# Optimization experiments

Hardware: AMD Instinct MI355X
Metric: run time of the kernel (lower is better)

Reference implementation:

```python
import jax, jax.numpy as jnp
import numpy as np

N = 100000   # nodes
E = 1600000  # edges (avg degree 16)
IN, H, OUT, P = 100, 256, 256, 128
EPS = 1e-5


def setup_inputs() -> dict:
    key = jax.random.key(0)
    ks = jax.random.split(key, 12)

    def lin(k, o, i):
        return jax.random.normal(k, (o, i), jnp.float32) / np.float32(np.sqrt(i))

    return {
        "x": jax.random.normal(ks[0], (N, IN), jnp.float32),
        "edge_index": jax.random.randint(ks[1], (2, E), 0, N),
        # SAGEConv l (aggregated-neighbor branch, has bias) and r (root branch, no bias)
        "Wl0": lin(ks[2], H, IN), "bl0": jnp.zeros((H,), jnp.float32), "Wr0": lin(ks[3], H, IN),
        "Wl1": lin(ks[4], H, H),  "bl1": jnp.zeros((H,), jnp.float32), "Wr1": lin(ks[5], H, H),
        "Wl2": lin(ks[6], OUT, H), "bl2": jnp.zeros((OUT,), jnp.float32), "Wr2": lin(ks[7], OUT, H),
        # projection head + BatchNorm1d(128)
        "Wp": lin(ks[8], P, OUT), "bp": jnp.zeros((P,), jnp.float32),
        "gamma": jnp.ones((P,), jnp.float32), "beta": jnp.zeros((P,), jnp.float32),
    }


def _sage_conv(x, src, dst, Wl, bl, Wr):
    # PyG SAGEConv default: mean-aggregate source features into destinations,
    # then lin_l(agg) + lin_r(x).
    agg = jax.ops.segment_sum(x[src], dst, num_segments=N)           # [N, d]
    deg = jax.ops.segment_sum(jnp.ones((src.shape[0],), x.dtype), dst, num_segments=N)
    agg = agg / jnp.maximum(deg, 1.0)[:, None]
    return agg @ Wl.T + bl + x @ Wr.T


def reference(x, edge_index, Wl0, bl0, Wr0, Wl1, bl1, Wr1, Wl2, bl2, Wr2, Wp, bp, gamma, beta):
    src, dst = edge_index[0], edge_index[1]
    x = jax.nn.relu(_sage_conv(x, src, dst, Wl0, bl0, Wr0))  # dropout is identity in eval
    x = jax.nn.relu(_sage_conv(x, src, dst, Wl1, bl1, Wr1))
    x = _sage_conv(x, src, dst, Wl2, bl2, Wr2)               # no relu on last layer
    z = x @ Wp.T + bp                                        # projection head -> [N, 128]
    mu = jnp.mean(z, axis=0)
    var = jnp.var(z, axis=0)                                 # biased, as torch BN uses for normalization
    h = gamma * (z - mu) * jax.lax.rsqrt(var + EPS) + beta
    return (x, h)
```

## Files before the change

### kernel.cpp

```cpp
#include <hip/hip_runtime.h>
#include <hip/hip_bf16.h>

#define EPS_BN 1e-5f

using short8  = __attribute__((ext_vector_type(8))) short;
using ushort8 = __attribute__((ext_vector_type(8))) unsigned short;
using f32x4   = __attribute__((ext_vector_type(4))) float;

__device__ inline float bf2f(unsigned short u) {
    union { unsigned i; float f; } c; c.i = ((unsigned)u) << 16; return c.f;
}
__device__ inline unsigned short f2bf(float f) {
    unsigned x = __float_as_uint(f);
    unsigned r = (x + 0x7FFF + ((x >> 16) & 1)) >> 16;
    return (unsigned short)r;
}

__global__ void zero_i32(int* __restrict__ p, int n) {
    int i = blockIdx.x * blockDim.x + threadIdx.x;
    if (i < n) p[i] = 0;
}
__global__ void zero_f32(float* __restrict__ p, int n) {
    int i = blockIdx.x * blockDim.x + threadIdx.x;
    if (i < n) p[i] = 0.0f;
}

__global__ void conv_w(const float* __restrict__ w, unsigned short* __restrict__ o,
                       int R, int C, int CP) {
    int t = blockIdx.x * blockDim.x + threadIdx.x;
    if (t >= R * CP) return;
    int r = t / CP, c = t % CP;
    o[t] = (c < C) ? f2bf(w[(size_t)r * C + c]) : (unsigned short)0;
}

__global__ void conv_x_pad(const float* __restrict__ x, unsigned short* __restrict__ xp, int n) {
    int t = blockIdx.x * blockDim.x + threadIdx.x;
    if (t >= n * 32) return;
    int node = t >> 5, g = t & 31;
    int f0 = g * 4;
    ushort4 o;
    const float* xr = x + (size_t)node * 100;
    o.x = (f0 + 0 < 100) ? f2bf(xr[f0 + 0]) : 0;
    o.y = (f0 + 1 < 100) ? f2bf(xr[f0 + 1]) : 0;
    o.z = (f0 + 2 < 100) ? f2bf(xr[f0 + 2]) : 0;
    o.w = (f0 + 3 < 100) ? f2bf(xr[f0 + 3]) : 0;
    *(ushort4*)(xp + (size_t)node * 128 + f0) = o;
}

__global__ void count_k(const int* __restrict__ dst, int* __restrict__ counts, int E) {
    int i = blockIdx.x * blockDim.x + threadIdx.x;
    if (i < E) atomicAdd(&counts[dst[i]], 1);
}

__global__ void scan1(const int* __restrict__ counts, int* __restrict__ rp,
                      int* __restrict__ partials, int n) {
    __shared__ int s[256];
    int t = threadIdx.x;
    int i = blockIdx.x * 256 + t;
    int v = (i < n) ? counts[i] : 0;
    s[t] = v;
    __syncthreads();
    for (int off = 1; off < 256; off <<= 1) {
        int u = (t >= off) ? s[t - off] : 0;
        __syncthreads();
        s[t] += u;
        __syncthreads();
    }
    if (i < n) rp[i] = s[t] - v;
    if (t == 255) partials[blockIdx.x] = s[255];
}

__global__ void scan2(int* __restrict__ partials, int nb) {
    __shared__ int s[512];
    int t = threadIdx.x;
    int v = (t < nb) ? partials[t] : 0;
    s[t] = v;
    __syncthreads();
    for (int off = 1; off < 512; off <<= 1) {
        int u = (t >= off) ? s[t - off] : 0;
        __syncthreads();
        s[t] += u;
        __syncthreads();
    }
    if (t < nb) partials[t] = s[t] - v;
}

__global__ void scan3(int* __restrict__ rp, const int* __restrict__ partials, int n, int E) {
    int i = blockIdx.x * blockDim.x + threadIdx.x;
    if (i < n) rp[i] += partials[i >> 8];
    if (i == 0) rp[n] = E;
}

__global__ void fill_k(const int* __restrict__ src, const int* __restrict__ dst,
                       const int* __restrict__ rp, int* __restrict__ cursor,
                       int* __restrict__ col, int E) {
    int i = blockIdx.x * blockDim.x + threadIdx.x;
    if (i < E) {
        int d = dst[i];
        int pos = atomicAdd(&cursor[d], 1);
        col[rp[d] + pos] = src[i];
    }
}

__global__ __launch_bounds__(256) void agg_bf16_256(
    const unsigned short* __restrict__ x, const int* __restrict__ rp,
    const int* __restrict__ col, unsigned short* __restrict__ out, int n) {
    int wave = threadIdx.x >> 6, lane = threadIdx.x & 63;
    int node = blockIdx.x * 4 + wave;
    if (node >= n) return;
    int s = rp[node], e = rp[node + 1];
    int deg = e - s;
    int h = lane >> 5;
    int l32 = lane & 31;

    float a[8] = {0, 0, 0, 0, 0, 0, 0, 0};
    int base = 0;
    for (; base + 8 <= deg; base += 8) {
        int i = s + base + h;
        int r0 = col[i], r1 = col[i + 2], r2 = col[i + 4], r3 = col[i + 6];
        ushort8 v0 = *(const ushort8*)(x + (size_t)r0 * 256 + l32 * 8);
        ushort8 v1 = *(const ushort8*)(x + (size_t)r1 * 256 + l32 * 8);
        ushort8 v2 = *(const ushort8*)(x + (size_t)r2 * 256 + l32 * 8);
        ushort8 v3 = *(const ushort8*)(x + (size_t)r3 * 256 + l32 * 8);
#pragma unroll
        for (int j = 0; j < 8; ++j)
            a[j] += bf2f(v0[j]) + bf2f(v1[j]) + bf2f(v2[j]) + bf2f(v3[j]);
    }
    for (int i = s + base + h; i < e; i += 2) {
        int r = col[i];
        ushort8 v = *(const ushort8*)(x + (size_t)r * 256 + l32 * 8);
#pragma unroll
        for (int j = 0; j < 8; ++j) a[j] += bf2f(v[j]);
    }
#pragma unroll
    for (int j = 0; j < 8; ++j) a[j] += __shfl_xor(a[j], 32);

    if (h == 0) {
        float sc = 1.0f / fmaxf((float)deg, 1.0f);
        ushort8 o;
#pragma unroll
        for (int j = 0; j < 8; ++j) o[j] = f2bf(a[j] * sc);
        *(ushort8*)(out + (size_t)node * 256 + l32 * 8) = o;
    }
}

__global__ __launch_bounds__(256) void agg_bf16_128(
    const unsigned short* __restrict__ x, const int* __restrict__ rp,
    const int* __restrict__ col, unsigned short* __restrict__ out, int n) {
    int wave = threadIdx.x >> 6, lane = threadIdx.x & 63;
    int node = blockIdx.x * 4 + wave;
    if (node >= n) return;
    int s = rp[node], e = rp[node + 1];
    int deg = e - s;
    int q = lane >> 4;
    int l16 = lane & 15;

    float a[8] = {0, 0, 0, 0, 0, 0, 0, 0};
    int base = 0;
    for (; base + 16 <= deg; base += 16) {
        int i = s + base + q;
        int r0 = col[i], r1 = col[i + 4], r2 = col[i + 8], r3 = col[i + 12];
        ushort8 v0 = *(const ushort8*)(x + (size_t)r0 * 128 + l16 * 8);
        ushort8 v1 = *(const ushort8*)(x + (size_t)r1 * 128 + l16 * 8);
        ushort8 v2 = *(const ushort8*)(x + (size_t)r2 * 128 + l16 * 8);
        ushort8 v3 = *(const ushort8*)(x + (size_t)r3 * 128 + l16 * 8);
#pragma unroll
        for (int j = 0; j < 8; ++j)
            a[j] += bf2f(v0[j]) + bf2f(v1[j]) + bf2f(v2[j]) + bf2f(v3[j]);
    }
    for (int i = s + base + q; i < e; i += 4) {
        int r = col[i];
        ushort8 v = *(const ushort8*)(x + (size_t)r * 128 + l16 * 8);
#pragma unroll
        for (int j = 0; j < 8; ++j) a[j] += bf2f(v[j]);
    }
#pragma unroll
    for (int j = 0; j < 8; ++j) {
        a[j] += __shfl_xor(a[j], 16);
        a[j] += __shfl_xor(a[j], 32);
    }

    if (lane < 16) {
        float sc = 1.0f / fmaxf((float)deg, 1.0f);
        ushort8 o;
#pragma unroll
        for (int j = 0; j < 8; ++j) o[j] = f2bf(a[j] * sc);
        *(ushort8*)(out + (size_t)node * 128 + l16 * 8) = o;
    }
}

template <int KTOT, int DOUT, bool HAS_AGG, bool RELU, bool STF32, bool STBF16>
__global__ __launch_bounds__(256) void sage_mfma(
    const unsigned short* __restrict__ xp, const unsigned short* __restrict__ ap,
    const unsigned short* __restrict__ Wr, const unsigned short* __restrict__ Wl,
    const float* __restrict__ bias,
    float* __restrict__ outf, unsigned short* __restrict__ outb, int n) {
    constexpr int CT = DOUT / 16;
    constexpr int NSRC = HAS_AGG ? 2 : 1;
    constexpr int FR = DOUT * 4;
    __shared__ __align__(16) unsigned short lds[NSRC * FR * 8];

    const int t = threadIdx.x;
    const int wave = t >> 6, lane = t & 63;
    const int node0 = blockIdx.x * 64 + wave * 16;
    const bool active = node0 < n;
    const int lcol = lane & 15, lq = lane >> 4;

    f32x4 acc[CT];
#pragma unroll
    for (int c = 0; c < CT; ++c) {
        float b = bias[c * 16 + lcol];
        acc[c][0] = b; acc[c][1] = b; acc[c][2] = b; acc[c][3] = b;
    }

    const unsigned short* aRow  = xp + (size_t)(node0 + lcol) * KTOT + lq * 8;
    const unsigned short* aRow2 = HAS_AGG ? (ap + (size_t)(node0 + lcol) * KTOT + lq * 8) : xp;

    for (int ks = 0; ks < KTOT / 32; ++ks) {
        for (int r = t; r < NSRC * FR; r += 256) {
            int srcSel = r / FR;
            int id = r % FR;
            int ct = id >> 6, l = id & 63;
            const unsigned short* W = (srcSel == 0) ? Wr : Wl;
            uint4 v = *(const uint4*)(W + (size_t)(ct * 16 + (l & 15)) * KTOT + ks * 32 + (l >> 4) * 8);
            *(uint4*)(lds + (size_t)r * 8) = v;
        }
        __syncthreads();
        if (active) {
            short8 a = *(const short8*)(aRow + ks * 32);
            short8 a2;
            if (HAS_AGG) a2 = *(const short8*)(aRow2 + ks * 32);
            const short8* bf = (const short8*)lds;
#pragma unroll
            for (int c = 0; c < CT; ++c)
                acc[c] = __builtin_amdgcn_mfma_f32_16x16x32_bf16(a, bf[c * 64 + lane], acc[c], 0, 0, 0);
            if (HAS_AGG) {
                const short8* bf2 = bf + FR;
#pragma unroll
                for (int c = 0; c < CT; ++c)
                    acc[c] = __builtin_amdgcn_mfma_f32_16x16x32_bf16(a2, bf2[c * 64 + lane], acc[c], 0, 0, 0);
            }
        }
        __syncthreads();
    }
    if (!active) return;

#pragma unroll
    for (int c = 0; c < CT; ++c) {
        f32x4 v = acc[c];
        if (RELU) {
            v[0] = fmaxf(v[0], 0.0f); v[1] = fmaxf(v[1], 0.0f);
            v[2] = fmaxf(v[2], 0.0f); v[3] = fmaxf(v[3], 0.0f);
        }
#pragma unroll
        for (int j = 0; j < 4; ++j) {
            size_t row = (size_t)node0 + lq * 4 + j;
            int colI = c * 16 + lcol;
            if (STF32) outf[row * DOUT + colI] = v[j];
            if (STBF16) outb[row * DOUT + colI] = f2bf(v[j]);
        }
    }
}

__global__ void bn_partial(const float* __restrict__ z, float* __restrict__ sums, int n) {
    int f = threadIdx.x & 127;
    int half = threadIdx.x >> 7;
    float s = 0.0f, s2 = 0.0f;
    for (int row = blockIdx.x * 2 + half; row < n; row += gridDim.x * 2) {
        float v = z[(size_t)row * 128 + f];
        s += v; s2 += v * v;
    }
    __shared__ float ls[256], ls2[256];
    ls[threadIdx.x] = s; ls2[threadIdx.x] = s2;
    __syncthreads();
    if (half == 0) {
        atomicAdd(&sums[f], s + ls[128 + f]);
        atomicAdd(&sums[128 + f], s2 + ls2[128 + f]);
    }
}

__global__ void bn_finalize(const float* __restrict__ sums, const float* __restrict__ gamma,
                            const float* __restrict__ beta, float* __restrict__ params, int n) {
    int f = threadIdx.x;
    float mu = sums[f] / (float)n;
    float var = sums[128 + f] / (float)n - mu * mu;
    float inv = rsqrtf(var + EPS_BN);
    float sc = gamma[f] * inv;
    params[f] = sc;
    params[128 + f] = beta[f] - mu * sc;
}

__global__ void bn_apply(float* __restrict__ z, const float* __restrict__ params, int total4) {
    int i = blockIdx.x * blockDim.x + threadIdx.x;
    for (; i < total4; i += gridDim.x * blockDim.x) {
        float4 v = ((float4*)z)[i];
        int f0 = (i & 31) * 4;
        v.x = v.x * params[f0 + 0] + params[128 + f0 + 0];
        v.y = v.y * params[f0 + 1] + params[128 + f0 + 1];
        v.z = v.z * params[f0 + 2] + params[128 + f0 + 2];
        v.w = v.w * params[f0 + 3] + params[128 + f0 + 3];
        ((float4*)z)[i] = v;
    }
}

extern "C" void kernel_launch(void* const* d_in, const int* in_sizes, int n_in,
                              void* d_out, int out_size, void* d_ws, size_t ws_size,
                              hipStream_t stream) {
    const float* x_in  = (const float*)d_in[0];
    const int*   ei    = (const int*)d_in[1];
    const float* Wl0   = (const float*)d_in[2];
    const float* bl0   = (const float*)d_in[3];
    const float* Wr0   = (const float*)d_in[4];
    const float* Wl1   = (const float*)d_in[5];
    const float* bl1   = (const float*)d_in[6];
    const float* Wr1   = (const float*)d_in[7];
    const float* Wl2   = (const float*)d_in[8];
    const float* bl2   = (const float*)d_in[9];
    const float* Wr2   = (const float*)d_in[10];
    const float* Wp    = (const float*)d_in[11];
    const float* bp    = (const float*)d_in[12];
    const float* gamma = (const float*)d_in[13];
    const float* beta  = (const float*)d_in[14];

    const int IN = 100, INP = 128, H = 256, OUT = 256, P = 128;
    const int n = in_sizes[0] / IN;
    const int E = in_sizes[1] / 2;
    const int* src = ei;
    const int* dst = ei + E;

    size_t off = 0;
    auto alloc = [&](size_t bytes) -> char* {
        char* p = (char*)d_ws + off;
        off += (bytes + 255) & ~(size_t)255;
        return p;
    };
    int*   counts   = (int*)alloc((size_t)n * 4);
    int*   cursor   = (int*)alloc((size_t)n * 4);
    int*   rp       = (int*)alloc((size_t)(n + 1) * 4);
    int*   partials = (int*)alloc(512 * 4);
    int*   col      = (int*)alloc((size_t)E * 4);
    unsigned short* Wl0b = (unsigned short*)alloc((size_t)H * INP * 2);
    unsigned short* Wr0b = (unsigned short*)alloc((size_t)H * INP * 2);
    unsigned short* Wl1b = (unsigned short*)alloc((size_t)H * H * 2);
    unsigned short* Wr1b = (unsigned short*)alloc((size_t)H * H * 2);
    unsigned short* Wl2b = (unsigned short*)alloc((size_t)OUT * H * 2);
    unsigned short* Wr2b = (unsigned short*)alloc((size_t)OUT * H * 2);
    unsigned short* Wpb  = (unsigned short*)alloc((size_t)P * OUT * 2);
    float* bnsums   = (float*)alloc(256 * 4);
    float* bnparams = (float*)alloc(256 * 4);
    unsigned short* bufA = (unsigned short*)alloc((size_t)n * H * 2);
    unsigned short* bufB = (unsigned short*)alloc((size_t)n * H * 2);
    unsigned short* bufC = (unsigned short*)alloc((size_t)n * H * 2);
    unsigned short* bufD = (unsigned short*)alloc((size_t)n * H * 2);

    unsigned short* xpad   = bufA;
    unsigned short* aggpad = bufA + (size_t)n * INP;
    unsigned short* h1b  = bufB;
    unsigned short* agg1 = bufC;
    unsigned short* h2b  = bufD;
    unsigned short* agg2 = bufB;
    unsigned short* xb2  = bufA;

    float* out_x = (float*)d_out;
    float* z     = out_x + (size_t)n * OUT;

    const int nb = (n + 255) / 256;
    const int gemm_grid = (n + 63) / 64;

    zero_i32<<<nb, 256, 0, stream>>>(counts, n);
    zero_i32<<<nb, 256, 0, stream>>>(cursor, n);
    zero_f32<<<1, 256, 0, stream>>>(bnsums, 256);
    count_k<<<(E + 255) / 256, 256, 0, stream>>>(dst, counts, E);
    scan1<<<nb, 256, 0, stream>>>(counts, rp, partials, n);
    scan2<<<1, 512, 0, stream>>>(partials, nb);
    scan3<<<nb, 256, 0, stream>>>(rp, partials, n, E);
    fill_k<<<(E + 255) / 256, 256, 0, stream>>>(src, dst, rp, cursor, col, E);

    conv_x_pad<<<(n * 32 + 255) / 256, 256, 0, stream>>>(x_in, xpad, n);
    conv_w<<<(H * INP + 255) / 256, 256, 0, stream>>>(Wl0, Wl0b, H, IN, INP);
    conv_w<<<(H * INP + 255) / 256, 256, 0, stream>>>(Wr0, Wr0b, H, IN, INP);
    conv_w<<<(H * H + 255) / 256, 256, 0, stream>>>(Wl1, Wl1b, H, H, H);
    conv_w<<<(H * H + 255) / 256, 256, 0, stream>>>(Wr1, Wr1b, H, H, H);
    conv_w<<<(OUT * H + 255) / 256, 256, 0, stream>>>(Wl2, Wl2b, OUT, H, H);
    conv_w<<<(OUT * H + 255) / 256, 256, 0, stream>>>(Wr2, Wr2b, OUT, H, H);
    conv_w<<<(P * OUT + 255) / 256, 256, 0, stream>>>(Wp, Wpb, P, OUT, OUT);

    agg_bf16_128<<<(n + 3) / 4, 256, 0, stream>>>(xpad, rp, col, aggpad, n);
    sage_mfma<128, 256, true, true, false, true><<<gemm_grid, 256, 0, stream>>>(
        xpad, aggpad, Wr0b, Wl0b, bl0, nullptr, h1b, n);

    agg_bf16_256<<<(n + 3) / 4, 256, 0, stream>>>(h1b, rp, col, agg1, n);
    sage_mfma<256, 256, true, true, false, true><<<gemm_grid, 256, 0, stream>>>(
        h1b, agg1, Wr1b, Wl1b, bl1, nullptr, h2b, n);

    agg_bf16_256<<<(n + 3) / 4, 256, 0, stream>>>(h2b, rp, col, agg2, n);
    sage_mfma<256, 256, true, false, true, true><<<gemm_grid, 256, 0, stream>>>(
        h2b, agg2, Wr2b, Wl2b, bl2, out_x, xb2, n);

    sage_mfma<256, 128, false, false, true, false><<<gemm_grid, 256, 0, stream>>>(
        xb2, nullptr, Wpb, nullptr, bp, z, nullptr, n);

    bn_partial<<<256, 256, 0, stream>>>(z, bnsums, n);
    bn_finalize<<<1, 128, 0, stream>>>(bnsums, gamma, beta, bnparams, n);
    bn_apply<<<2048, 256, 0, stream>>>(z, bnparams, n * (P / 4));
}
```

Measured before the change: 821.8 us.

## Double-buffer weight staging via direct global-to-LDS loads and 512-thread GEMM blocks

Rewrites the weight staging in the SAGE MFMA GEMM so each wave issues direct global-to-LDS loads into a double-buffered shared tile, prefetching the next k-slice while the current one is consumed. Blocks grow to 512 threads covering 128 nodes, which halves how often each weight slice is reloaded per node. It also defers the aggregate-row load until just before use. The loop still needs a sync before the next buffer is overwritten, and the larger LDS footprint (two buffers) may reduce occupancy.

```diff
diff --git a/kernel.cpp b/kernel.cpp
--- a/kernel.cpp
+++ b/kernel.cpp
@@ -6,6 +6,9 @@
 using short8  = __attribute__((ext_vector_type(8))) short;
 using ushort8 = __attribute__((ext_vector_type(8))) unsigned short;
 using f32x4   = __attribute__((ext_vector_type(4))) float;
+
+typedef const __attribute__((address_space(1))) void* gas_ptr;
+typedef __attribute__((address_space(3))) void* las_ptr;
 
 __device__ inline float bf2f(unsigned short u) {
     union { unsigned i; float f; } c; c.i = ((unsigned)u) << 16; return c.f;
@@ -190,21 +193,38 @@
 }
 
 template <int KTOT, int DOUT, bool HAS_AGG, bool RELU, bool STF32, bool STBF16>
-__global__ __launch_bounds__(256) void sage_mfma(
+__global__ __launch_bounds__(512) void sage_mfma(
     const unsigned short* __restrict__ xp, const unsigned short* __restrict__ ap,
     const unsigned short* __restrict__ Wr, const unsigned short* __restrict__ Wl,
     const float* __restrict__ bias,
     float* __restrict__ outf, unsigned short* __restrict__ outb, int n) {
     constexpr int CT = DOUT / 16;
     constexpr int NSRC = HAS_AGG ? 2 : 1;
-    constexpr int FR = DOUT * 4;
-    __shared__ __align__(16) unsigned short lds[NSRC * FR * 8];
+    constexpr int FR = NSRC == 2 ? DOUT * 4 : DOUT * 4;
+    constexpr int CHUNKS = NSRC * CT;
+    constexpr int CPW = CHUNKS / 8;
+    constexpr int KS = KTOT / 32;
+    constexpr int BUFSZ = NSRC * FR * 8;
+    __shared__ __align__(16) unsigned short lds[2 * BUFSZ];
 
     const int t = threadIdx.x;
     const int wave = t >> 6, lane = t & 63;
-    const int node0 = blockIdx.x * 64 + wave * 16;
+    const int node0 = blockIdx.x * 128 + wave * 16;
     const bool active = node0 < n;
     const int lcol = lane & 15, lq = lane >> 4;
+
+    auto stage = [&](int ks, int buf) {
+        unsigned short* base = lds + buf * BUFSZ;
+#pragma unroll
+        for (int i = 0; i < CPW; ++i) {
+            int chunk = wave * CPW + i;
+            int srcSel = chunk / CT, ct = chunk % CT;
+            const unsigned short* W = (srcSel == 0) ? Wr : Wl;
+            const unsigned short* g = W + (size_t)(ct * 16 + lcol) * KTOT + ks * 32 + lq * 8;
+            unsigned short* l = base + chunk * 512;
+            __builtin_amdgcn_global_load_lds((gas_ptr)g, (las_ptr)l, 16, 0, 0);
+        }
+    };
 
     f32x4 acc[CT];
 #pragma unroll
@@ -216,25 +236,19 @@
     const unsigned short* aRow  = xp + (size_t)(node0 + lcol) * KTOT + lq * 8;
     const unsigned short* aRow2 = HAS_AGG ? (ap + (size_t)(node0 + lcol) * KTOT + lq * 8) : xp;
 
-    for (int ks = 0; ks < KTOT / 32; ++ks) {
-        for (int r = t; r < NSRC * FR; r += 256) {
-            int srcSel = r / FR;
-            int id = r % FR;
-            int ct = id >> 6, l = id & 63;
-            const unsigned short* W = (srcSel == 0) ? Wr : Wl;
-            uint4 v = *(const uint4*)(W + (size_t)(ct * 16 + (l & 15)) * KTOT + ks * 32 + (l >> 4) * 8);
-            *(uint4*)(lds + (size_t)r * 8) = v;
-        }
-        __syncthreads();
+    stage(0, 0);
+    __syncthreads();
+
+    for (int ks = 0; ks < KS; ++ks) {
+        if (ks + 1 < KS) stage(ks + 1, (ks + 1) & 1);
         if (active) {
             short8 a = *(const short8*)(aRow + ks * 32);
-            short8 a2;
-            if (HAS_AGG) a2 = *(const short8*)(aRow2 + ks * 32);
-            const short8* bf = (const short8*)lds;
+            const short8* bf = (const short8*)(lds + (ks & 1) * BUFSZ);
 #pragma unroll
             for (int c = 0; c < CT; ++c)
                 acc[c] = __builtin_amdgcn_mfma_f32_16x16x32_bf16(a, bf[c * 64 + lane], acc[c], 0, 0, 0);
             if (HAS_AGG) {
+                short8 a2 = *(const short8*)(aRow2 + ks * 32);
                 const short8* bf2 = bf + FR;
 #pragma unroll
                 for (int c = 0; c < CT; ++c)
@@ -365,7 +379,7 @@
     float* z     = out_x + (size_t)n * OUT;
 
     const int nb = (n + 255) / 256;
-    const int gemm_grid = (n + 63) / 64;
+    const int gemm_grid = (n + 127) / 128;
 
     zero_i32<<<nb, 256, 0, stream>>>(counts, n);
     zero_i32<<<nb, 256, 0, stream>>>(cursor, n);
@@ -386,18 +400,18 @@
     conv_w<<<(P * OUT + 255) / 256, 256, 0, stream>>>(Wp, Wpb, P, OUT, OUT);
 
     agg_bf16_128<<<(n + 3) / 4, 256, 0, stream>>>(xpad, rp, col, aggpad, n);
-    sage_mfma<128, 256, true, true, false, true><<<gemm_grid, 256, 0, stream>>>(
+    sage_mfma<128, 256, true, true, false, true><<<gemm_grid, 512, 0, stream>>>(
         xpad, aggpad, Wr0b, Wl0b, bl0, nullptr, h1b, n);
 
     agg_bf16_256<<<(n + 3) / 4, 256, 0, stream>>>(h1b, rp, col, agg1, n);
-    sage_mfma<256, 256, true, true, false, true><<<gemm_grid, 256, 0, stream>>>(
+    sage_mfma<256, 256, true, true, false, true><<<gemm_grid, 512, 0, stream>>>(
         h1b, agg1, Wr1b, Wl1b, bl1, nullptr, h2b, n);
 
     agg_bf16_256<<<(n + 3) / 4, 256, 0, stream>>>(h2b, rp, col, agg2, n);
-    sage_mfma<256, 256, true, false, true, true><<<gemm_grid, 256, 0, stream>>>(
+    sage_mfma<256, 256, true, false, true, true><<<gemm_grid, 512, 0, stream>>>(
         h2b, agg2, Wr2b, Wl2b, bl2, out_x, xb2, n);
 
-    sage_mfma<256, 128, false, false, true, false><<<gemm_grid, 256, 0, stream>>>(
+    sage_mfma<256, 128, false, false, true, false><<<gemm_grid, 512, 0, stream>>>(
         xb2, nullptr, Wpb, nullptr, bp, z, nullptr, n);
 
     bn_partial<<<256, 256, 0, stream>>>(z, bnsums, n);
```

Measured after the change: 742.4 us. -9.7%, faster.

## Register-tile SAGE GEMMs with 64x64 per-wave tiles and double-buffered direct loads

Applied to the files above, without the earlier changes.

Replaces the LDS-staged weight GEMM, where each wave computed a 16-row strip across all output columns, with 512-thread blocks in which each wave owns a 64x64 output tile. A and B fragments are loaded straight from global memory into registers and double-buffered across k-steps, which removes the shared-memory staging and both __syncthreads per k-step. The aim is more MFMA work per loaded fragment and fewer block-level barriers. In exchange, register pressure is much higher (16 accumulators plus two sets of operand fragments), weights are read repeatedly from global or L2 memory, and occupancy may drop.

```diff
diff --git a/kernel.cpp b/kernel.cpp
--- a/kernel.cpp
+++ b/kernel.cpp
@@ -189,75 +189,106 @@
     }
 }
 
-template <int KTOT, int DOUT, bool HAS_AGG, bool RELU, bool STF32, bool STBF16>
-__global__ __launch_bounds__(256) void sage_mfma(
+template <int KTOT, int DOUT, bool HAS_AGG, bool RELU, bool STF32, bool STBF16, int WAVES_M>
+__global__ __launch_bounds__(512) void sage_mfma(
     const unsigned short* __restrict__ xp, const unsigned short* __restrict__ ap,
     const unsigned short* __restrict__ Wr, const unsigned short* __restrict__ Wl,
     const float* __restrict__ bias,
     float* __restrict__ outf, unsigned short* __restrict__ outb, int n) {
-    constexpr int CT = DOUT / 16;
-    constexpr int NSRC = HAS_AGG ? 2 : 1;
-    constexpr int FR = DOUT * 4;
-    __shared__ __align__(16) unsigned short lds[NSRC * FR * 8];
+    constexpr int WAVES_N = 8 / WAVES_M;
+    constexpr int KS = KTOT / 32;
+    static_assert(DOUT / 16 / WAVES_N == 4, "wave owns 4 col tiles");
 
     const int t = threadIdx.x;
     const int wave = t >> 6, lane = t & 63;
-    const int node0 = blockIdx.x * 64 + wave * 16;
-    const bool active = node0 < n;
+    const int wm = wave / WAVES_N, wn = wave % WAVES_N;
     const int lcol = lane & 15, lq = lane >> 4;
-
-    f32x4 acc[CT];
-#pragma unroll
-    for (int c = 0; c < CT; ++c) {
-        float b = bias[c * 16 + lcol];
-        acc[c][0] = b; acc[c][1] = b; acc[c][2] = b; acc[c][3] = b;
-    }
-
-    const unsigned short* aRow  = xp + (size_t)(node0 + lcol) * KTOT + lq * 8;
-    const unsigned short* aRow2 = HAS_AGG ? (ap + (size_t)(node0 + lcol) * KTOT + lq * 8) : xp;
-
-    for (int ks = 0; ks < KTOT / 32; ++ks) {
-        for (int r = t; r < NSRC * FR; r += 256) {
-            int srcSel = r / FR;
-            int id = r % FR;
-            int ct = id >> 6, l = id & 63;
-            const unsigned short* W = (srcSel == 0) ? Wr : Wl;
-            uint4 v = *(const uint4*)(W + (size_t)(ct * 16 + (l & 15)) * KTOT + ks * 32 + (l >> 4) * 8);
-            *(uint4*)(lds + (size_t)r * 8) = v;
+    const int node_base = blockIdx.x * (WAVES_M * 64) + wm * 64;
+    const int col0 = wn * 64;
+
+    f32x4 acc[4][4];
+#pragma unroll
+    for (int ct = 0; ct < 4; ++ct) {
+        float b = bias[col0 + ct * 16 + lcol];
+#pragma unroll
+        for (int mt = 0; mt < 4; ++mt) {
+            acc[mt][ct][0] = b; acc[mt][ct][1] = b; acc[mt][ct][2] = b; acc[mt][ct][3] = b;
         }
-        __syncthreads();
-        if (active) {
-            short8 a = *(const short8*)(aRow + ks * 32);
-            short8 a2;
-            if (HAS_AGG) a2 = *(const short8*)(aRow2 + ks * 32);
-            const short8* bf = (const short8*)lds;
-#pragma unroll
-            for (int c = 0; c < CT; ++c)
-                acc[c] = __builtin_amdgcn_mfma_f32_16x16x32_bf16(a, bf[c * 64 + lane], acc[c], 0, 0, 0);
-            if (HAS_AGG) {
-                const short8* bf2 = bf + FR;
-#pragma unroll
-                for (int c = 0; c < CT; ++c)
-                    acc[c] = __builtin_amdgcn_mfma_f32_16x16x32_bf16(a2, bf2[c * 64 + lane], acc[c], 0, 0, 0);
+    }
+
+    const unsigned short* aPx[4];
+    const unsigned short* aPa[4];
+    const unsigned short* bPr[4];
+    const unsigned short* bPl[4];
+#pragma unroll
+    for (int i = 0; i < 4; ++i) {
+        aPx[i] = xp + (size_t)(node_base + i * 16 + lcol) * KTOT + lq * 8;
+        bPr[i] = Wr + (size_t)(col0 + i * 16 + lcol) * KTOT + lq * 8;
+        if (HAS_AGG) {
+            aPa[i] = ap + (size_t)(node_base + i * 16 + lcol) * KTOT + lq * 8;
+            bPl[i] = Wl + (size_t)(col0 + i * 16 + lcol) * KTOT + lq * 8;
+        }
+    }
+
+    short8 axE[4], aaE[4], brE[4], blE[4];
+    short8 axO[4], aaO[4], brO[4], blO[4];
+
+    auto LOAD = [&](int ks, short8 (&ax)[4], short8 (&aa)[4],
+                    short8 (&br)[4], short8 (&bl)[4]) {
+#pragma unroll
+        for (int i = 0; i < 4; ++i) {
+            ax[i] = *(const short8*)(aPx[i] + ks * 32);
+            br[i] = *(const short8*)(bPr[i] + ks * 32);
+        }
+        if constexpr (HAS_AGG) {
+#pragma unroll
+            for (int i = 0; i < 4; ++i) {
+                aa[i] = *(const short8*)(aPa[i] + ks * 32);
+                bl[i] = *(const short8*)(bPl[i] + ks * 32);
             }
         }
-        __syncthreads();
-    }
-    if (!active) return;
-
-#pragma unroll
-    for (int c = 0; c < CT; ++c) {
-        f32x4 v = acc[c];
-        if (RELU) {
-            v[0] = fmaxf(v[0], 0.0f); v[1] = fmaxf(v[1], 0.0f);
-            v[2] = fmaxf(v[2], 0.0f); v[3] = fmaxf(v[3], 0.0f);
-        }
-#pragma unroll
-        for (int j = 0; j < 4; ++j) {
-            size_t row = (size_t)node0 + lq * 4 + j;
-            int colI = c * 16 + lcol;
-            if (STF32) outf[row * DOUT + colI] = v[j];
-            if (STBF16) outb[row * DOUT + colI] = f2bf(v[j]);
+    };
+    auto MM = [&](short8 (&ax)[4], short8 (&aa)[4],
+                  short8 (&br)[4], short8 (&bl)[4]) {
+#pragma unroll
+        for (int mt = 0; mt < 4; ++mt)
+#pragma unroll
+            for (int ct = 0; ct < 4; ++ct) {
+                acc[mt][ct] = __builtin_amdgcn_mfma_f32_16x16x32_bf16(
+                    ax[mt], br[ct], acc[mt][ct], 0, 0, 0);
+                if constexpr (HAS_AGG)
+                    acc[mt][ct] = __builtin_amdgcn_mfma_f32_16x16x32_bf16(
+                        aa[mt], bl[ct], acc[mt][ct], 0, 0, 0);
+            }
+    };
+
+    LOAD(0, axE, aaE, brE, blE);
+#pragma unroll
+    for (int ks = 0; ks < KS; ks += 2) {
+        LOAD(ks + 1, axO, aaO, brO, blO);
+        MM(axE, aaE, brE, blE);
+        if (ks + 2 < KS) LOAD(ks + 2, axE, aaE, brE, blE);
+        MM(axO, aaO, brO, blO);
+    }
+
+#pragma unroll
+    for (int mt = 0; mt < 4; ++mt) {
+        int nb0 = node_base + mt * 16;
+        if (nb0 >= n) continue;
+#pragma unroll
+        for (int ct = 0; ct < 4; ++ct) {
+            f32x4 v = acc[mt][ct];
+            if (RELU) {
+                v[0] = fmaxf(v[0], 0.0f); v[1] = fmaxf(v[1], 0.0f);
+                v[2] = fmaxf(v[2], 0.0f); v[3] = fmaxf(v[3], 0.0f);
+            }
+            int colI = col0 + ct * 16 + lcol;
+#pragma unroll
+            for (int j = 0; j < 4; ++j) {
+                size_t row = (size_t)nb0 + lq * 4 + j;
+                if (STF32) outf[row * DOUT + colI] = v[j];
+                if (STBF16) outb[row * DOUT + colI] = f2bf(v[j]);
+            }
         }
     }
 }
@@ -352,6 +383,7 @@
     unsigned short* bufB = (unsigned short*)alloc((size_t)n * H * 2);
     unsigned short* bufC = (unsigned short*)alloc((size_t)n * H * 2);
     unsigned short* bufD = (unsigned short*)alloc((size_t)n * H * 2);
+    (void)alloc((size_t)256 * 512);
 
     unsigned short* xpad   = bufA;
     unsigned short* aggpad = bufA + (size_t)n * INP;
@@ -365,7 +397,6 @@
     float* z     = out_x + (size_t)n * OUT;
 
     const int nb = (n + 255) / 256;
-    const int gemm_grid = (n + 63) / 64;
 
     zero_i32<<<nb, 256, 0, stream>>>(counts, n);
     zero_i32<<<nb, 256, 0, stream>>>(cursor, n);
@@ -386,18 +417,18 @@
     conv_w<<<(P * OUT + 255) / 256, 256, 0, stream>>>(Wp, Wpb, P, OUT, OUT);
 
     agg_bf16_128<<<(n + 3) / 4, 256, 0, stream>>>(xpad, rp, col, aggpad, n);
-    sage_mfma<128, 256, true, true, false, true><<<gemm_grid, 256, 0, stream>>>(
+    sage_mfma<128, 256, true, true, false, true, 2><<<(n + 127) / 128, 512, 0, stream>>>(
         xpad, aggpad, Wr0b, Wl0b, bl0, nullptr, h1b, n);
 
     agg_bf16_256<<<(n + 3) / 4, 256, 0, stream>>>(h1b, rp, col, agg1, n);
-    sage_mfma<256, 256, true, true, false, true><<<gemm_grid, 256, 0, stream>>>(
+    sage_mfma<256, 256, true, true, false, true, 2><<<(n + 127) / 128, 512, 0, stream>>>(
         h1b, agg1, Wr1b, Wl1b, bl1, nullptr, h2b, n);
 
     agg_bf16_256<<<(n + 3) / 4, 256, 0, stream>>>(h2b, rp, col, agg2, n);
-    sage_mfma<256, 256, true, false, true, true><<<gemm_grid, 256, 0, stream>>>(
+    sage_mfma<256, 256, true, false, true, true, 2><<<(n + 127) / 128, 512, 0, stream>>>(
         h2b, agg2, Wr2b, Wl2b, bl2, out_x, xb2, n);
 
-    sage_mfma<256, 128, false, false, true, false><<<gemm_grid, 256, 0, stream>>>(
+    sage_mfma<256, 128, false, false, true, false, 4><<<(n + 255) / 256, 512, 0, stream>>>(
         xb2, nullptr, Wpb, nullptr, bp, z, nullptr, n);
 
     bn_partial<<<256, 256, 0, stream>>>(z, bnsums, n);
```

Measured after the change: 912.9 us. 1.11x slower.
